# Kernel tuning notes

Hardware: AMD Instinct MI355X
Metric: run time of the kernel (lower is better)

## Reference

```python
import jax, jax.numpy as jnp
import numpy as np

T, N, C = 4096, 16, 512


def setup_inputs() -> dict:
    key = jax.random.key(0)
    k1, k2, k3 = jax.random.split(key, 3)
    x = jax.random.normal(k1, (T, N, C), dtype=jnp.float32)
    cached_len = jax.random.randint(k2, (N,), 0, 1000, dtype=jnp.int32)
    cached_avg = jax.random.normal(k3, (N, C), dtype=jnp.float32)
    return {"x": x, "cached_len": cached_len, "cached_avg": cached_avg}


def reference(x, cached_len, cached_avg):
    # x: (T, N, C); cached_len: (N,) int; cached_avg: (N, C)
    t = x.shape[0]
    len_f = cached_len.astype(x.dtype)  # (N,)
    # running sum including cached state
    csum = jnp.cumsum(x, axis=0) + (cached_avg * len_f[:, None])[None]  # (T,N,C)
    # per-step counts: arange(1..T) + cached_len, broadcast to (T, N, 1)
    counts = jnp.arange(1, t + 1, dtype=x.dtype)[:, None] + len_f[None, :]  # (T,N)
    new_x = csum * (1.0 / counts)[:, :, None]  # (T,N,C)
    new_cached_len = cached_len + t
    new_cached_avg = new_x[-1]
    return new_x, new_cached_len, new_cached_avg
```

## Files before the change

kernel.cpp:

```cpp
#include <hip/hip_runtime.h>

constexpr int T      = 4096;
constexpr int N      = 16;
constexpr int C      = 512;
constexpr int NC     = N * C;
constexpr int NC4    = NC / 4;
constexpr int CH     = 64;
constexpr int L      = T / CH;
constexpr int TNC    = T * NC;
constexpr int STRIPS = NC4 / 256;

__global__ __launch_bounds__(256) void pool_k1_sums(
    const float* __restrict__ x, float* __restrict__ partial)
{
    int gid  = blockIdx.x * blockDim.x + threadIdx.x;
    int ch   = gid >> 11;
    int col4 = gid & (NC4 - 1);

    const float4* xp = reinterpret_cast<const float4*>(x);
    float4 s = make_float4(0.f, 0.f, 0.f, 0.f);
    int base = ch * L * NC4 + col4;
#pragma unroll 8
    for (int i = 0; i < L; ++i) {
        float4 v = xp[base + i * NC4];
        s.x += v.x; s.y += v.y; s.z += v.z; s.w += v.w;
    }
    reinterpret_cast<float4*>(partial)[ch * NC4 + col4] = s;
}

__global__ __launch_bounds__(256) void pool_k2_scan(
    const float* __restrict__ x,
    const float* __restrict__ partial,
    const int* __restrict__ cached_len,
    const float* __restrict__ cached_avg,
    float* __restrict__ out,
    float* __restrict__ out_len,
    float* __restrict__ out_avg)
{
    int blk   = blockIdx.x;
    int ch    = blk >> 3;
    int strip = blk & (STRIPS - 1);
    int col4  = strip * 256 + threadIdx.x;
    int n     = col4 >> 7;
    float lenf = (float)cached_len[n];

    const float4* pp = reinterpret_cast<const float4*>(partial);
    float4 s = make_float4(0.f, 0.f, 0.f, 0.f);
#pragma unroll 8
    for (int j = 0; j < ch; ++j) {
        float4 v = pp[j * NC4 + col4];
        s.x += v.x; s.y += v.y; s.z += v.z; s.w += v.w;
    }

    float4 b = reinterpret_cast<const float4*>(cached_avg)[col4];
    b.x *= lenf; b.y *= lenf; b.z *= lenf; b.w *= lenf;

    const float4* xp = reinterpret_cast<const float4*>(x);
    float4* op = reinterpret_cast<float4*>(out);

    int t0 = ch * L;
    float4 o = make_float4(0.f, 0.f, 0.f, 0.f);
#pragma unroll 8
    for (int i = 0; i < L; ++i) {
        int t = t0 + i;
        float4 v = xp[t * NC4 + col4];
        s.x += v.x; s.y += v.y; s.z += v.z; s.w += v.w;
        float r = 1.0f / ((float)(t + 1) + lenf);
        o.x = (s.x + b.x) * r;
        o.y = (s.y + b.y) * r;
        o.z = (s.z + b.z) * r;
        o.w = (s.w + b.w) * r;
        op[t * NC4 + col4] = o;
    }

    if (ch == CH - 1) {
        reinterpret_cast<float4*>(out_avg)[col4] = o;
    }
    if (blk == 0 && threadIdx.x < N) {
        out_len[threadIdx.x] = (float)(cached_len[threadIdx.x] + T);
    }
}

extern "C" void kernel_launch(void* const* d_in, const int* in_sizes, int n_in,
                              void* d_out, int out_size, void* d_ws, size_t ws_size,
                              hipStream_t stream)
{
    const float* x          = (const float*)d_in[0];
    const int*   cached_len = (const int*)d_in[1];
    const float* cached_avg = (const float*)d_in[2];

    float* out     = (float*)d_out;
    float* out_len = out + TNC;
    float* out_avg = out + TNC + N;

    float* partial = (float*)d_ws;

    pool_k1_sums<<<CH * NC4 / 256, 256, 0, stream>>>(x, partial);
    pool_k2_scan<<<CH * STRIPS,    256, 0, stream>>>(x, partial, cached_len, cached_avg,
                                                     out, out_len, out_avg);
}
```

Measured before the change: 262.5 us.

## Replace two-pass scan with single-pass decoupled look-back scan

Merges the partial-sum kernel and the scan kernel into one kernel that uses a decoupled look-back: each block publishes its aggregate and inclusive prefix through flags in workspace, and later blocks walk back to assemble their exclusive prefix. Each block keeps its 64-row tile in registers, so x is read once instead of twice and the pass over the partial-sum array disappears. In exchange it adds a memset, spin-waiting on global flags and a reliance on blocks being scheduled roughly in order. A bounded spin count could silently produce wrong prefixes if blocks stall.

```diff
diff --git a/kernel.cpp b/kernel.cpp
--- a/kernel.cpp
+++ b/kernel.cpp
@@ -1,71 +1,116 @@
 #include <hip/hip_runtime.h>
 
-constexpr int T      = 4096;
-constexpr int N      = 16;
-constexpr int C      = 512;
-constexpr int NC     = N * C;
-constexpr int NC4    = NC / 4;
-constexpr int CH     = 64;
-constexpr int L      = T / CH;
-constexpr int TNC    = T * NC;
-constexpr int STRIPS = NC4 / 256;
+constexpr int T    = 4096;
+constexpr int N    = 16;
+constexpr int C    = 512;
+constexpr int NC   = N * C;
+constexpr int NC4  = NC / 4;
+constexpr int TNC  = T * NC;
 
-__global__ __launch_bounds__(256) void pool_k1_sums(
-    const float* __restrict__ x, float* __restrict__ partial)
+constexpr int RB   = 64;
+constexpr int CB   = 64;
+constexpr int RT   = 16;
+constexpr int NCH  = T / RB;
+constexpr int NST  = NC4 / CB;
+constexpr int NBLK = NCH * NST;
+
+__device__ __forceinline__ void acc(float4& a, const float4& b) {
+    a.x += b.x; a.y += b.y; a.z += b.z; a.w += b.w;
+}
+
+__global__ __launch_bounds__(256) void pool_scan(
+    const float* __restrict__ x,
+    const int*   __restrict__ cached_len,
+    const float* __restrict__ cached_avg,
+    float*       __restrict__ out,
+    float*       __restrict__ out_len,
+    float*       __restrict__ out_avg,
+    int*         __restrict__ flag_agg,
+    int*         __restrict__ flag_incl,
+    float4*      __restrict__ vagg,
+    float4*      __restrict__ vincl)
 {
-    int gid  = blockIdx.x * blockDim.x + threadIdx.x;
-    int ch   = gid >> 11;
-    int col4 = gid & (NC4 - 1);
+    const int bid   = blockIdx.x;
+    const int ch    = bid >> 5;
+    const int strip = bid & (NST - 1);
+    const int rg    = threadIdx.x >> 6;
+    const int col   = threadIdx.x & 63;
+    const int col4  = strip * CB + col;
+    const int row0  = ch * RB + rg * RT;
+    const int nIdx  = col4 >> 7;
+    const float lenf = (float)cached_len[nIdx];
+
+    __shared__ float4 xch[4][CB];
+    __shared__ float4 exch[CB];
 
     const float4* xp = reinterpret_cast<const float4*>(x);
-    float4 s = make_float4(0.f, 0.f, 0.f, 0.f);
-    int base = ch * L * NC4 + col4;
-#pragma unroll 8
-    for (int i = 0; i < L; ++i) {
-        float4 v = xp[base + i * NC4];
-        s.x += v.x; s.y += v.y; s.z += v.z; s.w += v.w;
-    }
-    reinterpret_cast<float4*>(partial)[ch * NC4 + col4] = s;
-}
-
-__global__ __launch_bounds__(256) void pool_k2_scan(
-    const float* __restrict__ x,
-    const float* __restrict__ partial,
-    const int* __restrict__ cached_len,
-    const float* __restrict__ cached_avg,
-    float* __restrict__ out,
-    float* __restrict__ out_len,
-    float* __restrict__ out_avg)
-{
-    int blk   = blockIdx.x;
-    int ch    = blk >> 3;
-    int strip = blk & (STRIPS - 1);
-    int col4  = strip * 256 + threadIdx.x;
-    int n     = col4 >> 7;
-    float lenf = (float)cached_len[n];
-
-    const float4* pp = reinterpret_cast<const float4*>(partial);
-    float4 s = make_float4(0.f, 0.f, 0.f, 0.f);
-#pragma unroll 8
-    for (int j = 0; j < ch; ++j) {
-        float4 v = pp[j * NC4 + col4];
-        s.x += v.x; s.y += v.y; s.z += v.z; s.w += v.w;
+    float4 v[RT];
+    float4 sum = make_float4(0.f, 0.f, 0.f, 0.f);
+#pragma unroll
+    for (int i = 0; i < RT; ++i) {
+        v[i] = xp[(row0 + i) * NC4 + col4];
+        acc(sum, v[i]);
     }
 
+    xch[rg][col] = sum;
+    __syncthreads();
+    float4 rgpre = make_float4(0.f, 0.f, 0.f, 0.f);
+#pragma unroll
+    for (int r = 0; r < 3; ++r)
+        if (r < rg) acc(rgpre, xch[r][col]);
+
+    if (rg == 0) {
+        float4 tot = xch[0][col];
+        acc(tot, xch[1][col]); acc(tot, xch[2][col]); acc(tot, xch[3][col]);
+        vagg[bid * CB + col] = tot;
+        __threadfence();
+        if (threadIdx.x == 0)
+            __hip_atomic_store(&flag_agg[bid], 1, __ATOMIC_RELEASE,
+                               __HIP_MEMORY_SCOPE_AGENT);
+
+        float4 excl = make_float4(0.f, 0.f, 0.f, 0.f);
+        int walk = ch - 1;
+        int spin = 0;
+        while (walk >= 0) {
+            const int sidx = walk * NST + strip;
+            if (__hip_atomic_load(&flag_incl[sidx], __ATOMIC_ACQUIRE,
+                                  __HIP_MEMORY_SCOPE_AGENT)) {
+                acc(excl, vincl[sidx * CB + col]);
+                break;
+            }
+            if (__hip_atomic_load(&flag_agg[sidx], __ATOMIC_ACQUIRE,
+                                  __HIP_MEMORY_SCOPE_AGENT)) {
+                acc(excl, vagg[sidx * CB + col]);
+                --walk;
+                continue;
+            }
+            __builtin_amdgcn_s_sleep(8);
+            if (++spin > (1 << 22)) break;
+        }
+
+        float4 incl = excl;
+        acc(incl, tot);
+        vincl[bid * CB + col] = incl;
+        __threadfence();
+        if (threadIdx.x == 0)
+            __hip_atomic_store(&flag_incl[bid], 1, __ATOMIC_RELEASE,
+                               __HIP_MEMORY_SCOPE_AGENT);
+        exch[col] = excl;
+    }
+    __syncthreads();
+
+    float4 s = exch[col];
+    acc(s, rgpre);
     float4 b = reinterpret_cast<const float4*>(cached_avg)[col4];
     b.x *= lenf; b.y *= lenf; b.z *= lenf; b.w *= lenf;
 
-    const float4* xp = reinterpret_cast<const float4*>(x);
     float4* op = reinterpret_cast<float4*>(out);
-
-    int t0 = ch * L;
     float4 o = make_float4(0.f, 0.f, 0.f, 0.f);
-#pragma unroll 8
-    for (int i = 0; i < L; ++i) {
-        int t = t0 + i;
-        float4 v = xp[t * NC4 + col4];
-        s.x += v.x; s.y += v.y; s.z += v.z; s.w += v.w;
-        float r = 1.0f / ((float)(t + 1) + lenf);
+#pragma unroll
+    for (int i = 0; i < RT; ++i) {
+        acc(s, v[i]);
+        const int t = row0 + i;
+        const float r = 1.0f / ((float)(t + 1) + lenf);
         o.x = (s.x + b.x) * r;
         o.y = (s.y + b.y) * r;
         o.z = (s.z + b.z) * r;
@@ -73,12 +118,10 @@
         op[t * NC4 + col4] = o;
     }
 
-    if (ch == CH - 1) {
+    if (ch == NCH - 1 && rg == 3)
         reinterpret_cast<float4*>(out_avg)[col4] = o;
-    }
-    if (blk == 0 && threadIdx.x < N) {
+    if (bid == 0 && threadIdx.x < N)
         out_len[threadIdx.x] = (float)(cached_len[threadIdx.x] + T);
-    }
 }
 
 extern "C" void kernel_launch(void* const* d_in, const int* in_sizes, int n_in,
@@ -93,9 +136,15 @@
     float* out_len = out + TNC;
     float* out_avg = out + TNC + N;
 
-    float* partial = (float*)d_ws;
+    char* ws = (char*)d_ws;
+    int*    flag_agg  = (int*)ws;
+    int*    flag_incl = (int*)(ws + 8192);
+    float4* vagg      = (float4*)(ws + 16384);
+    float4* vincl     = (float4*)(ws + 16384 + (size_t)NBLK * CB * 16);
 
-    pool_k1_sums<<<CH * NC4 / 256, 256, 0, stream>>>(x, partial);
-    pool_k2_scan<<<CH * STRIPS,    256, 0, stream>>>(x, partial, cached_len, cached_avg,
-                                                     out, out_len, out_avg);
+    hipMemsetAsync(d_ws, 0, 16384, stream);
+
+    pool_scan<<<NBLK, 256, 0, stream>>>(x, cached_len, cached_avg,
+                                        out, out_len, out_avg,
+                                        flag_agg, flag_incl, vagg, vincl);
 }
```

Result: slower. 688.7 us (+162.4%).
